# Kernel tuning notes

Hardware: AMD Instinct MI355X
Metric: run time of the kernel (lower is better)

## Reference

```python
import jax, jax.numpy as jnp
import numpy as np

HEADS = 16
DIM_HEAD = 128
SCALE = DIM_HEAD ** -0.5


def rotate_half(x):
    # x: (..., d) with d even; pairs (x1, x2) -> (-x2, x1)
    x = x.reshape(*x.shape[:-1], -1, 2)
    x1, x2 = x[..., 0], x[..., 1]
    return jnp.stack([-x2, x1], axis=-1).reshape(*x.shape[:-2], -1)


def apply_rotary(freqs, t):
    # freqs: (n, d), t: (b, h, n, d)
    cos = jnp.cos(freqs)[None, None]
    sin = jnp.sin(freqs)[None, None]
    return t * cos + rotate_half(t) * sin


def setup_inputs() -> dict:
    key = jax.random.key(0)
    ks = jax.random.split(key, 6)
    b, n, dim = 2, 2048, 2048
    inner = HEADS * DIM_HEAD
    s = dim ** -0.5
    x = jax.random.normal(ks[0], (b, n, dim), dtype=jnp.float32)
    rotary_emb = jax.random.normal(ks[1], (n, DIM_HEAD), dtype=jnp.float32)
    Wq = jax.random.normal(ks[2], (dim, inner), dtype=jnp.float32) * s
    Wkv = jax.random.normal(ks[3], (dim, 2 * inner), dtype=jnp.float32) * s
    Wo = jax.random.normal(ks[4], (inner, dim), dtype=jnp.float32) * s
    bo = jnp.zeros((dim,), dtype=jnp.float32)
    return {"x": x, "rotary_emb": rotary_emb, "Wq": Wq, "Wkv": Wkv, "Wo": Wo, "bo": bo}


def reference(x, rotary_emb, Wq, Wkv, Wo, bo):
    b, n, _ = x.shape
    q = x @ Wq                      # (b, n, inner)
    kv = x @ Wkv                    # (b, n, 2*inner)
    k, v = jnp.split(kv, 2, axis=-1)
    # b n (h d) -> b h n d
    split = lambda t: t.reshape(b, n, HEADS, DIM_HEAD).transpose(0, 2, 1, 3)
    q, k, v = split(q), split(k), split(v)
    q = apply_rotary(rotary_emb, q)
    k = apply_rotary(rotary_emb, k)
    q = q * SCALE
    dots = jnp.einsum('bhid,bhjd->bhij', q, k)
    attn = jax.nn.softmax(dots, axis=-1)
    out = jnp.einsum('bhij,bhjd->bhid', attn, v)
    out = out.transpose(0, 2, 1, 3).reshape(b, n, HEADS * DIM_HEAD)
    return out @ Wo + bo
```

## Files before the change

### kernel.cpp

```cpp
#include <hip/hip_runtime.h>
#include <stdint.h>

typedef __attribute__((ext_vector_type(8))) short s16x8;
typedef __attribute__((ext_vector_type(4))) float f32x4;

#define DEVFN static __device__ __forceinline__

constexpr int   S_LEN = 2048;
constexpr int   DH    = 128;
constexpr int   INNER = 2048;
constexpr float ASCALE = 0.08838834764831845f;

DEVFN float b2f(unsigned short u) {
  union { unsigned int i; float f; } v; v.i = ((unsigned int)u) << 16; return v.f;
}
DEVFN unsigned short f2b(float f) {
  union { float f; unsigned int i; } v; v.f = f;
  unsigned int r = v.i + 0x7fffu + ((v.i >> 16) & 1u);
  return (unsigned short)(r >> 16);
}
DEVFN void async_cp16(const unsigned short* g, unsigned short* l) {
  __builtin_amdgcn_global_load_lds((const __attribute__((address_space(1))) void*)g,
                                   (__attribute__((address_space(3))) void*)l, 16, 0, 0);
}

__global__ __launch_bounds__(256) void cvt_bf16_k(const float* __restrict__ in,
                                                  unsigned short* __restrict__ out) {
  const size_t e = ((size_t)blockIdx.x * 256 + threadIdx.x) * 8;
  const float4 a = *(const float4*)(in + e);
  const float4 b = *(const float4*)(in + e + 4);
  union { s16x8 v; unsigned short u[8]; } o;
  o.u[0] = f2b(a.x); o.u[1] = f2b(a.y); o.u[2] = f2b(a.z); o.u[3] = f2b(a.w);
  o.u[4] = f2b(b.x); o.u[5] = f2b(b.y); o.u[6] = f2b(b.z); o.u[7] = f2b(b.w);
  *(s16x8*)(out + e) = o.v;
}

__global__ __launch_bounds__(256) void rot_cs_k(const float* __restrict__ rot,
                                                float2* __restrict__ cst) {
  const int idx = blockIdx.x * 256 + threadIdx.x;
  const float f = rot[idx];
  float s, c;
  __sincosf(f, &s, &c);
  cst[idx] = make_float2(c, s);
}

__global__ __launch_bounds__(256) void transpose_cvt_k(const float* __restrict__ in,
                                                       unsigned short* __restrict__ out,
                                                       int R, int C) {
  __shared__ __align__(16) unsigned short tile[64][72];
  const int t  = threadIdx.x;
  const int lr = t >> 3;
  const int lc = (t & 7) << 3;
  const size_t ibase = (size_t)blockIdx.y * 64 * C + (size_t)blockIdx.x * 64;
#pragma unroll
  for (int rr = 0; rr < 64; rr += 32) {
    const float* p = in + ibase + (size_t)(rr + lr) * C + lc;
    const float4 a = *(const float4*)p;
    const float4 b = *(const float4*)(p + 4);
    unsigned short* tp = &tile[rr + lr][lc];
    tp[0] = f2b(a.x); tp[1] = f2b(a.y); tp[2] = f2b(a.z); tp[3] = f2b(a.w);
    tp[4] = f2b(b.x); tp[5] = f2b(b.y); tp[6] = f2b(b.z); tp[7] = f2b(b.w);
  }
  __syncthreads();
  const size_t obase = (size_t)blockIdx.x * 64 * R + (size_t)blockIdx.y * 64;
#pragma unroll
  for (int rr = 0; rr < 64; rr += 32) {
    int oc = rr + lr;
    union { s16x8 v; unsigned short s[8]; } u;
#pragma unroll
    for (int j = 0; j < 8; ++j) u.s[j] = tile[lc + j][oc];
    *(s16x8*)(out + obase + (size_t)oc * R + lc) = u.v;
  }
}

template <int EPI>
__global__ __launch_bounds__(256) void gemm_bt(
    const unsigned short* __restrict__ A,
    const unsigned short* __restrict__ Bt,
    unsigned short* __restrict__ out0,
    unsigned short* __restrict__ out1,
    unsigned short* __restrict__ out2,
    float* __restrict__ outf,
    const float* __restrict__ biasf,
    const float2* __restrict__ rotcs,
    int M, int N, int K) {
  __shared__ __align__(16) unsigned short smem[16384];
  unsigned short* As = smem;
  unsigned short* Bs = smem + 8192;
  const int tid  = threadIdx.x;
  const int wave = tid >> 6, lane = tid & 63;
  const int wm = wave & 1, wn = wave >> 1;
  const int quad = lane >> 4, l15 = lane & 15;
  const int l7 = l15 & 7;
  const int m0 = blockIdx.x * 128, n0 = blockIdx.y * 128;

  f32x4 acc[4][4];
#pragma unroll
  for (int i = 0; i < 4; ++i)
#pragma unroll
    for (int j = 0; j < 4; ++j) acc[i][j] = {0.f, 0.f, 0.f, 0.f};

  const int lrow = lane >> 3;
  const int lchk = (lane & 7) ^ (lrow & 7);
  const unsigned short* a_g = A  + (size_t)(m0 + wave * 32 + lrow) * K + (lchk << 3);
  const unsigned short* b_g = Bt + (size_t)(n0 + wave * 32 + lrow) * K + (lchk << 3);
  unsigned short* As_w = As + (wave * 32) * 64;
  unsigned short* Bs_w = Bs + (wave * 32) * 64;

  for (int k0 = 0; k0 < K; k0 += 64) {
    __syncthreads();
#pragma unroll
    for (int t = 0; t < 4; ++t) {
      async_cp16(a_g + k0 + (size_t)(t * 8) * K, As_w + t * 8 * 64);
      async_cp16(b_g + k0 + (size_t)(t * 8) * K, Bs_w + t * 8 * 64);
    }
    __syncthreads();
#pragma unroll
    for (int ks = 0; ks < 2; ++ks) {
      s16x8 af[4], bfr[4];
#pragma unroll
      for (int mi = 0; mi < 4; ++mi)
        af[mi] = *(const s16x8*)(As + (wm * 64 + mi * 16 + l15) * 64 + (((ks * 4 + quad) ^ l7) << 3));
#pragma unroll
      for (int ni = 0; ni < 4; ++ni)
        bfr[ni] = *(const s16x8*)(Bs + (wn * 64 + ni * 16 + l15) * 64 + (((ks * 4 + quad) ^ l7) << 3));
#pragma unroll
      for (int mi = 0; mi < 4; ++mi)
#pragma unroll
        for (int ni = 0; ni < 4; ++ni)
          acc[mi][ni] = __builtin_amdgcn_mfma_f32_16x16x32_bf16(af[mi], bfr[ni], acc[mi][ni], 0, 0, 0);
    }
  }

  if constexpr (EPI == 1) {
#pragma unroll
    for (int mi = 0; mi < 4; ++mi)
#pragma unroll
      for (int ni = 0; ni < 4; ++ni)
#pragma unroll
        for (int r = 0; r < 4; ++r) {
          const int gm = m0 + wm * 64 + mi * 16 + quad * 4 + r;
          const int gn = n0 + wn * 64 + ni * 16 + l15;
          outf[(size_t)gm * N + gn] = acc[mi][ni][r] + biasf[gn];
        }
  } else {
    __syncthreads();
    const int b     = m0 >> 11;
    const int ibase = m0 & 2047;
    if (n0 < 2 * INNER) {
      const bool isq = (n0 < INNER);
      const int h = (n0 & (INNER - 1)) >> 7;
#pragma unroll
      for (int mi = 0; mi < 4; ++mi)
#pragma unroll
        for (int ni = 0; ni < 4; ++ni) {
          const int dd = wn * 64 + ni * 16 + l15;
          const int ch = dd >> 3;
#pragma unroll
          for (int r = 0; r < 4; ++r) {
            const int il = wm * 64 + mi * 16 + quad * 4 + r;
            const float v  = acc[mi][ni][r];
            const float vp = __shfl_xor(v, 1);
            const float2 cs = rotcs[(size_t)(ibase + il) * 128 + dd];
            float rv = (dd & 1) ? fmaf(v, cs.x,  vp * cs.y)
                                : fmaf(v, cs.x, -vp * cs.y);
            if (isq) rv *= ASCALE;
            smem[il * 128 + ((ch ^ (il & 7)) << 3) + (dd & 7)] = f2b(rv);
          }
        }
      __syncthreads();
      unsigned short* outp = (isq ? out0 : out1) +
                             ((size_t)((b << 4) + h) * S_LEN + ibase) * DH;
#pragma unroll
      for (int it = 0; it < 8; ++it) {
        const int f  = it * 256 + tid;
        const int il = f >> 4, ch = f & 15;
        s16x8 vv = *(const s16x8*)(smem + il * 128 + ((ch ^ (il & 7)) << 3));
        *(s16x8*)(outp + (size_t)il * DH + (ch << 3)) = vv;
      }
    } else {
      const int h = (n0 - 2 * INNER) >> 7;
#pragma unroll
      for (int mi = 0; mi < 4; ++mi)
#pragma unroll
        for (int ni = 0; ni < 4; ++ni) {
          const int dd = wn * 64 + ni * 16 + l15;
#pragma unroll
          for (int r = 0; r < 4; ++r) {
            const int il = wm * 64 + mi * 16 + quad * 4 + r;
            smem[dd * 128 + (((il >> 3) ^ (dd & 7)) << 3) + (il & 7)] = f2b(acc[mi][ni][r]);
          }
        }
      __syncthreads();
      unsigned short* outp = out2 + (size_t)((b << 4) + h) * DH * S_LEN + ibase;
#pragma unroll
      for (int it = 0; it < 8; ++it) {
        const int f  = it * 256 + tid;
        const int dd = f >> 4, ch = f & 15;
        s16x8 vv = *(const s16x8*)(smem + dd * 128 + ((ch ^ (dd & 7)) << 3));
        *(s16x8*)(outp + (size_t)dd * S_LEN + (ch << 3)) = vv;
      }
    }
  }
}

DEVFN void stage_tile(const unsigned short* kh, const unsigned short* vh,
                      int j0, unsigned short* KsB, unsigned short* VsB, int tid) {
#pragma unroll
  for (int v = 0; v < 4; ++v) {
    const int off = v * 2048 + tid * 8;
    const int kr = off >> 7;
    const int kc = (((off & 127) >> 3) ^ (kr & 7)) << 3;
    async_cp16(kh + (size_t)(j0 + kr) * DH + kc, KsB + off);
    const int vr = off >> 6;
    const int vc = (((off & 63) >> 3) ^ (vr & 7)) << 3;
    async_cp16(vh + (size_t)vr * S_LEN + j0 + vc, VsB + off);
  }
}

__global__ __launch_bounds__(256, 2) void flash_attn(
    const unsigned short* __restrict__ q,
    const unsigned short* __restrict__ k,
    const unsigned short* __restrict__ vt,
    unsigned short* __restrict__ aout) {
  __shared__ __align__(16) unsigned short Ks[2][64 * 128];
  __shared__ __align__(16) unsigned short Vs[2][128 * 64];
  __shared__ __align__(16) unsigned short Ps[4][32 * 64];
  const int tid = threadIdx.x;
  const int w = tid >> 6, lane = tid & 63;
  const int quad = lane >> 4, l15 = lane & 15;
  const int l7 = l15 & 7;

  const int lin  = blockIdx.y * 16 + blockIdx.x;
  const int xcd  = lin & 7, slot = lin >> 3;
  const int bh   = (xcd << 2) + (slot >> 4);
  const int i0   = (slot & 15) * 128;

  const unsigned short* qh = q  + (size_t)bh * S_LEN * DH;
  const unsigned short* kh = k  + (size_t)bh * S_LEN * DH;
  const unsigned short* vh = vt + (size_t)bh * DH * S_LEN;

  s16x8 qf[2][4];
#pragma unroll
  for (int mi = 0; mi < 2; ++mi)
#pragma unroll
    for (int ks = 0; ks < 4; ++ks)
      qf[mi][ks] = *(const s16x8*)(qh + (size_t)(i0 + w * 32 + mi * 16 + l15) * DH + ks * 32 + quad * 8);

  f32x4 oacc[2][8];
#pragma unroll
  for (int mi = 0; mi < 2; ++mi)
#pragma unroll
    for (int ni = 0; ni < 8; ++ni) oacc[mi][ni] = {0.f, 0.f, 0.f, 0.f};
  float mrun[2][4], lrun[2][4];
#pragma unroll
  for (int mi = 0; mi < 2; ++mi)
#pragma unroll
    for (int r = 0; r < 4; ++r) { mrun[mi][r] = -1e30f; lrun[mi][r] = 0.f; }

  unsigned short* Pw = Ps[w];

  stage_tile(kh, vh, 0, Ks[0], Vs[0], tid);
  __syncthreads();
  int cur = 0;

  for (int j0 = 0; j0 < S_LEN; j0 += 64) {
    if (j0 + 64 < S_LEN)
      stage_tile(kh, vh, j0 + 64, Ks[cur ^ 1], Vs[cur ^ 1], tid);
    const unsigned short* Ksc = Ks[cur];
    const unsigned short* Vsc = Vs[cur];

    f32x4 sacc[2][4];
#pragma unroll
    for (int mi = 0; mi < 2; ++mi)
#pragma unroll
      for (int ni = 0; ni < 4; ++ni) sacc[mi][ni] = {0.f, 0.f, 0.f, 0.f};
#pragma unroll
    for (int ks = 0; ks < 4; ++ks) {
      s16x8 kb[4];
#pragma unroll
      for (int ni = 0; ni < 4; ++ni)
        kb[ni] = *(const s16x8*)(Ksc + (ni * 16 + l15) * 128 + (((ks * 4 + quad) ^ l7) << 3));
#pragma unroll
      for (int mi = 0; mi < 2; ++mi)
#pragma unroll
        for (int ni = 0; ni < 4; ++ni)
          sacc[mi][ni] = __builtin_amdgcn_mfma_f32_16x16x32_bf16(qf[mi][ks], kb[ni], sacc[mi][ni], 0, 0, 0);
    }

    float al[2][4];
    int anyresc = 0;
#pragma unroll
    for (int mi = 0; mi < 2; ++mi)
#pragma unroll
      for (int r = 0; r < 4; ++r) {
        float v = fmaxf(fmaxf(sacc[mi][0][r], sacc[mi][1][r]),
                        fmaxf(sacc[mi][2][r], sacc[mi][3][r]));
        v = fmaxf(v, __shfl_xor(v, 1));
        v = fmaxf(v, __shfl_xor(v, 2));
        v = fmaxf(v, __shfl_xor(v, 4));
        v = fmaxf(v, __shfl_xor(v, 8));
        const float mo   = mrun[mi][r];
        const int   resc = v > mo + 8.f;
        const float mnew = resc ? v : mo;
        const float a    = resc ? __expf(mo - v) : 1.f;
        mrun[mi][r] = mnew;
        al[mi][r]   = a;
        anyresc |= resc;
        float s0 = 0.f;
#pragma unroll
        for (int ni = 0; ni < 4; ++ni) {
          float p = __expf(sacc[mi][ni][r] - mnew);
          sacc[mi][ni][r] = p;
          s0 += p;
        }
        lrun[mi][r] = lrun[mi][r] * a + s0;
      }
    if (__any(anyresc)) {
#pragma unroll
      for (int mi = 0; mi < 2; ++mi)
#pragma unroll
        for (int ni = 0; ni < 8; ++ni)
#pragma unroll
          for (int r = 0; r < 4; ++r) oacc[mi][ni][r] *= al[mi][r];
    }

#pragma unroll
    for (int mi = 0; mi < 2; ++mi)
#pragma unroll
      for (int ni = 0; ni < 4; ++ni) {
        const int col = ni * 16 + l15;
        const int ch  = col >> 3;
#pragma unroll
        for (int r = 0; r < 4; ++r) {
          const int row = mi * 16 + quad * 4 + r;
          Pw[row * 64 + ((ch ^ (row & 7)) << 3) + (col & 7)] = f2b(sacc[mi][ni][r]);
        }
      }
    __threadfence_block();

#pragma unroll
    for (int ks = 0; ks < 2; ++ks) {
      const int swz = ((ks * 4 + quad) ^ l7) << 3;
      s16x8 pf[2];
#pragma unroll
      for (int mi = 0; mi < 2; ++mi)
        pf[mi] = *(const s16x8*)(Pw + (mi * 16 + l15) * 64 + swz);
#pragma unroll
      for (int ni = 0; ni < 8; ++ni) {
        s16x8 vb = *(const s16x8*)(Vsc + (ni * 16 + l15) * 64 + swz);
#pragma unroll
        for (int mi = 0; mi < 2; ++mi)
          oacc[mi][ni] = __builtin_amdgcn_mfma_f32_16x16x32_bf16(pf[mi], vb, oacc[mi][ni], 0, 0, 0);
      }
    }

    __syncthreads();
    cur ^= 1;
  }

  const int b = bh >> 4, h = bh & 15;
#pragma unroll
  for (int mi = 0; mi < 2; ++mi)
#pragma unroll
    for (int r = 0; r < 4; ++r) {
      float l = lrun[mi][r];
      l += __shfl_xor(l, 1);
      l += __shfl_xor(l, 2);
      l += __shfl_xor(l, 4);
      l += __shfl_xor(l, 8);
      const float inv = 1.0f / l;
      const int i = i0 + w * 32 + mi * 16 + quad * 4 + r;
#pragma unroll
      for (int ni = 0; ni < 8; ++ni) {
        const int dd = ni * 16 + l15;
        aout[((size_t)b * S_LEN + i) * INNER + h * DH + dd] = f2b(oacc[mi][ni][r] * inv);
      }
    }
}

extern "C" void kernel_launch(void* const* d_in, const int* in_sizes, int n_in,
                              void* d_out, int out_size, void* d_ws, size_t ws_size,
                              hipStream_t stream) {
  const float* x   = (const float*)d_in[0];
  const float* rot = (const float*)d_in[1];
  const float* Wq  = (const float*)d_in[2];
  const float* Wkv = (const float*)d_in[3];
  const float* Wo  = (const float*)d_in[4];
  const float* bo  = (const float*)d_in[5];
  float* out = (float*)d_out;

  unsigned short* ws = (unsigned short*)d_ws;
  unsigned short* wt  = ws;
  unsigned short* wot = wt  + (size_t)6144 * 2048;
  unsigned short* qb  = wot + (size_t)2048 * 2048;
  unsigned short* kb  = qb  + (size_t)32 * 2048 * 128;
  unsigned short* vtb = kb  + (size_t)32 * 2048 * 128;
  unsigned short* xb  = vtb + (size_t)32 * 2048 * 128;
  unsigned short* att = wt;

  float2* cst = (float2*)d_out;

  rot_cs_k<<<dim3(1024), 256, 0, stream>>>(rot, cst);
  cvt_bf16_k<<<dim3(4096), 256, 0, stream>>>(x, xb);
  transpose_cvt_k<<<dim3(32, 32), 256, 0, stream>>>(Wq,  wt, 2048, 2048);
  transpose_cvt_k<<<dim3(64, 32), 256, 0, stream>>>(Wkv, wt + (size_t)2048 * 2048, 2048, 4096);
  transpose_cvt_k<<<dim3(32, 32), 256, 0, stream>>>(Wo,  wot, 2048, 2048);

  gemm_bt<0><<<dim3(32, 48), 256, 0, stream>>>(xb, wt, qb, kb, vtb, nullptr, nullptr, cst, 4096, 6144, 2048);
  flash_attn<<<dim3(16, 32), 256, 0, stream>>>(qb, kb, vtb, att);
  gemm_bt<1><<<dim3(32, 16), 256, 0, stream>>>(att, wot, nullptr, nullptr, nullptr, out, bo, nullptr, 4096, 2048, 2048);
}
```

Measured before the change: 438.1 us.

## Add 256x256-tile pipelined QKV GEMM with block swizzle and async double buffering

Replaces the 128x128 QKV projection GEMM with a dedicated 512-thread kernel that computes 256x256 output tiles. It double-buffers A and B in 128 KB of LDS via async global-to-LDS copies, interleaves prefetch with MFMA phases under explicit barriers, raises wave priority around the MFMAs, and remaps block indices for L2 locality. The larger tile cuts global traffic per FLOP. In exchange it uses much more LDS and registers, which lowers occupancy, and it launches only 384 blocks, which may leave compute units unevenly loaded. The rotary and transposed-V epilogues are adapted to span two heads per tile.

```diff
diff --git a/kernel.cpp b/kernel.cpp
--- a/kernel.cpp
+++ b/kernel.cpp
@@ -73,16 +73,170 @@
   }
 }
 
-template <int EPI>
-__global__ __launch_bounds__(256) void gemm_bt(
+__global__ __launch_bounds__(512, 2) void gemm256_qkv(
     const unsigned short* __restrict__ A,
     const unsigned short* __restrict__ Bt,
     unsigned short* __restrict__ out0,
     unsigned short* __restrict__ out1,
     unsigned short* __restrict__ out2,
+    const float2* __restrict__ rotcs) {
+  constexpr int K = 2048, NT = 32;
+  __shared__ __align__(16) unsigned short smem[65536];
+  const int tid = threadIdx.x;
+  const int wid = tid >> 6, lane = tid & 63;
+  const int wm = wid >> 2, wn = wid & 3;
+  const int quad = lane >> 4, l15 = lane & 15, l7 = l15 & 7;
+
+  const int lin = blockIdx.x;
+  const int logical = (lin & 7) * 48 + (lin >> 3);
+  const int m0 = (logical & 15) * 256;
+  const int n0 = (logical >> 4) * 256;
+
+  const int r0 = tid >> 3, c0 = tid & 7;
+
+  f32x4 acc[8][4];
+#pragma unroll
+  for (int i = 0; i < 8; ++i)
+#pragma unroll
+    for (int j = 0; j < 4; ++j) acc[i][j] = {0.f, 0.f, 0.f, 0.f};
+
+  auto stageA = [&](int t, int h) {
+#pragma unroll
+    for (int s = 0; s < 2; ++s) {
+      const int r = s * 64 + r0;
+      async_cp16(A + (size_t)(m0 + h * 128 + r) * K + t * 64 + ((c0 ^ (r0 & 7)) << 3),
+                 smem + ((t & 1) * 2 + h) * 8192 + s * 4096 + tid * 8);
+    }
+  };
+  auto stageB = [&](int t, int h) {
+#pragma unroll
+    for (int s = 0; s < 2; ++s) {
+      const int r = s * 64 + r0;
+      async_cp16(Bt + (size_t)(n0 + h * 128 + r) * K + t * 64 + ((c0 ^ (r0 & 7)) << 3),
+                 smem + 32768 + ((t & 1) * 2 + h) * 8192 + s * 4096 + tid * 8);
+    }
+  };
+
+  stageA(0, 0); stageA(0, 1); stageB(0, 0); stageB(0, 1);
+  stageB(1, 0); stageB(1, 1);
+  asm volatile("s_waitcnt vmcnt(4)" ::: "memory");
+  __builtin_amdgcn_s_barrier();
+
+#pragma unroll 2
+  for (int t = 0; t < NT; ++t) {
+    const int cur = t & 1;
+    const unsigned short* Ab = smem + (cur * 2 + wm) * 8192;
+    const unsigned short* Bb = smem + 32768 + (cur * 2 + (wn >> 1)) * 8192;
+    const int bln = (wn & 1) * 64;
+    s16x8 bf[4][2];
+#pragma unroll
+    for (int p = 0; p < 4; ++p) {
+      s16x8 af[2][2];
+#pragma unroll
+      for (int j = 0; j < 2; ++j)
+#pragma unroll
+        for (int kk = 0; kk < 2; ++kk)
+          af[j][kk] = *(const s16x8*)(Ab + ((2 * p + j) * 16 + l15) * 64 + (((kk * 4 + quad) ^ l7) << 3));
+      if (p == 0) {
+#pragma unroll
+        for (int nf = 0; nf < 4; ++nf)
+#pragma unroll
+          for (int kk = 0; kk < 2; ++kk)
+            bf[nf][kk] = *(const s16x8*)(Bb + (bln + nf * 16 + l15) * 64 + (((kk * 4 + quad) ^ l7) << 3));
+      }
+      if (p == 0 && t + 1 < NT) stageA(t + 1, 0);
+      if (p == 1 && t + 1 < NT) stageA(t + 1, 1);
+      if (p == 2 && t + 2 < NT) stageB(t + 2, 0);
+      if (p == 3 && t + 2 < NT) stageB(t + 2, 1);
+      __builtin_amdgcn_s_barrier();
+      asm volatile("s_waitcnt lgkmcnt(0)" ::: "memory");
+      __builtin_amdgcn_sched_barrier(0);
+      __builtin_amdgcn_s_setprio(1);
+#pragma unroll
+      for (int kk = 0; kk < 2; ++kk)
+#pragma unroll
+        for (int j = 0; j < 2; ++j)
+#pragma unroll
+          for (int nf = 0; nf < 4; ++nf)
+            acc[2 * p + j][nf] = __builtin_amdgcn_mfma_f32_16x16x32_bf16(af[j][kk], bf[nf][kk], acc[2 * p + j][nf], 0, 0, 0);
+      __builtin_amdgcn_s_setprio(0);
+      __builtin_amdgcn_sched_barrier(0);
+      if (p == 3) {
+        if (t == NT - 2)      asm volatile("s_waitcnt vmcnt(0)" ::: "memory");
+        else if (t < NT - 2)  asm volatile("s_waitcnt vmcnt(4)" ::: "memory");
+      }
+      __builtin_amdgcn_s_barrier();
+    }
+  }
+
+  __syncthreads();
+  const int b = m0 >> 11, ibase = m0 & 2047;
+  if (n0 < 2 * INNER) {
+    const bool isq = (n0 < INNER);
+    const int hbase = (n0 & (INNER - 1)) >> 7;
+#pragma unroll
+    for (int mf = 0; mf < 8; ++mf)
+#pragma unroll
+      for (int nf = 0; nf < 4; ++nf) {
+        const int jl = wn * 64 + nf * 16 + l15;
+        const int dd = jl & 127;
+        const int cl = jl >> 3;
+#pragma unroll
+        for (int r = 0; r < 4; ++r) {
+          const int il = wm * 128 + mf * 16 + quad * 4 + r;
+          const float v  = acc[mf][nf][r];
+          const float vp = __shfl_xor(v, 1);
+          const float2 cs = rotcs[(size_t)(ibase + il) * 128 + dd];
+          float rv = (dd & 1) ? fmaf(v, cs.x,  vp * cs.y)
+                              : fmaf(v, cs.x, -vp * cs.y);
+          if (isq) rv *= ASCALE;
+          smem[il * 256 + ((cl ^ (il & 7)) << 3) + (jl & 7)] = f2b(rv);
+        }
+      }
+    __syncthreads();
+    unsigned short* outp = (isq ? out0 : out1) +
+                           ((size_t)((b << 4) + hbase) * S_LEN + ibase) * DH;
+#pragma unroll
+    for (int it = 0; it < 16; ++it) {
+      const int f  = it * 512 + tid;
+      const int il = f >> 5, cl = f & 31;
+      s16x8 vv = *(const s16x8*)(smem + il * 256 + ((cl ^ (il & 7)) << 3));
+      const int hh = cl >> 4, dd0 = (cl & 15) << 3;
+      *(s16x8*)(outp + (size_t)hh * S_LEN * DH + (size_t)il * DH + dd0) = vv;
+    }
+  } else {
+    const int hbase = (n0 - 2 * INNER) >> 7;
+#pragma unroll
+    for (int mf = 0; mf < 8; ++mf)
+#pragma unroll
+      for (int nf = 0; nf < 4; ++nf) {
+        const int jl = wn * 64 + nf * 16 + l15;
+#pragma unroll
+        for (int r = 0; r < 4; ++r) {
+          const int il = wm * 128 + mf * 16 + quad * 4 + r;
+          const int ci = il >> 3;
+          smem[jl * 256 + ((ci ^ (jl & 7)) << 3) + (il & 7)] = f2b(acc[mf][nf][r]);
+        }
+      }
+    __syncthreads();
+    unsigned short* outp = out2 + (size_t)((b << 4) + hbase) * DH * S_LEN + ibase;
+#pragma unroll
+    for (int it = 0; it < 16; ++it) {
+      const int f  = it * 512 + tid;
+      const int jl = f >> 5, ci = f & 31;
+      s16x8 vv = *(const s16x8*)(smem + jl * 256 + ((ci ^ (jl & 7)) << 3));
+      const int hh = jl >> 7, dd = jl & 127;
+      *(s16x8*)(outp + (size_t)hh * DH * S_LEN + (size_t)dd * S_LEN + (ci << 3)) = vv;
+    }
+  }
+}
+
+template <int EPI>
+__global__ __launch_bounds__(256) void gemm_bt(
+    const unsigned short* __restrict__ A,
+    const unsigned short* __restrict__ Bt,
     float* __restrict__ outf,
     const float* __restrict__ biasf,
-    const float2* __restrict__ rotcs,
     int M, int N, int K) {
   __shared__ __align__(16) unsigned short smem[16384];
   unsigned short* As = smem;
@@ -132,76 +286,16 @@
     }
   }
 
-  if constexpr (EPI == 1) {
-#pragma unroll
-    for (int mi = 0; mi < 4; ++mi)
-#pragma unroll
-      for (int ni = 0; ni < 4; ++ni)
-#pragma unroll
-        for (int r = 0; r < 4; ++r) {
-          const int gm = m0 + wm * 64 + mi * 16 + quad * 4 + r;
-          const int gn = n0 + wn * 64 + ni * 16 + l15;
-          outf[(size_t)gm * N + gn] = acc[mi][ni][r] + biasf[gn];
-        }
-  } else {
-    __syncthreads();
-    const int b     = m0 >> 11;
-    const int ibase = m0 & 2047;
-    if (n0 < 2 * INNER) {
-      const bool isq = (n0 < INNER);
-      const int h = (n0 & (INNER - 1)) >> 7;
-#pragma unroll
-      for (int mi = 0; mi < 4; ++mi)
-#pragma unroll
-        for (int ni = 0; ni < 4; ++ni) {
-          const int dd = wn * 64 + ni * 16 + l15;
-          const int ch = dd >> 3;
-#pragma unroll
-          for (int r = 0; r < 4; ++r) {
-            const int il = wm * 64 + mi * 16 + quad * 4 + r;
-            const float v  = acc[mi][ni][r];
-            const float vp = __shfl_xor(v, 1);
-            const float2 cs = rotcs[(size_t)(ibase + il) * 128 + dd];
-            float rv = (dd & 1) ? fmaf(v, cs.x,  vp * cs.y)
-                                : fmaf(v, cs.x, -vp * cs.y);
-            if (isq) rv *= ASCALE;
-            smem[il * 128 + ((ch ^ (il & 7)) << 3) + (dd & 7)] = f2b(rv);
-          }
-        }
-      __syncthreads();
-      unsigned short* outp = (isq ? out0 : out1) +
-                             ((size_t)((b << 4) + h) * S_LEN + ibase) * DH;
-#pragma unroll
-      for (int it = 0; it < 8; ++it) {
-        const int f  = it * 256 + tid;
-        const int il = f >> 4, ch = f & 15;
-        s16x8 vv = *(const s16x8*)(smem + il * 128 + ((ch ^ (il & 7)) << 3));
-        *(s16x8*)(outp + (size_t)il * DH + (ch << 3)) = vv;
-      }
-    } else {
-      const int h = (n0 - 2 * INNER) >> 7;
-#pragma unroll
-      for (int mi = 0; mi < 4; ++mi)
-#pragma unroll
-        for (int ni = 0; ni < 4; ++ni) {
-          const int dd = wn * 64 + ni * 16 + l15;
-#pragma unroll
-          for (int r = 0; r < 4; ++r) {
-            const int il = wm * 64 + mi * 16 + quad * 4 + r;
-            smem[dd * 128 + (((il >> 3) ^ (dd & 7)) << 3) + (il & 7)] = f2b(acc[mi][ni][r]);
-          }
-        }
-      __syncthreads();
-      unsigned short* outp = out2 + (size_t)((b << 4) + h) * DH * S_LEN + ibase;
-#pragma unroll
-      for (int it = 0; it < 8; ++it) {
-        const int f  = it * 256 + tid;
-        const int dd = f >> 4, ch = f & 15;
-        s16x8 vv = *(const s16x8*)(smem + dd * 128 + ((ch ^ (dd & 7)) << 3));
-        *(s16x8*)(outp + (size_t)dd * S_LEN + (ch << 3)) = vv;
-      }
-    }
-  }
+#pragma unroll
+  for (int mi = 0; mi < 4; ++mi)
+#pragma unroll
+    for (int ni = 0; ni < 4; ++ni)
+#pragma unroll
+      for (int r = 0; r < 4; ++r) {
+        const int gm = m0 + wm * 64 + mi * 16 + quad * 4 + r;
+        const int gn = n0 + wn * 64 + ni * 16 + l15;
+        outf[(size_t)gm * N + gn] = acc[mi][ni][r] + biasf[gn];
+      }
 }
 
 DEVFN void stage_tile(const unsigned short* kh, const unsigned short* vh,
@@ -407,7 +501,7 @@
   transpose_cvt_k<<<dim3(64, 32), 256, 0, stream>>>(Wkv, wt + (size_t)2048 * 2048, 2048, 4096);
   transpose_cvt_k<<<dim3(32, 32), 256, 0, stream>>>(Wo,  wot, 2048, 2048);
 
-  gemm_bt<0><<<dim3(32, 48), 256, 0, stream>>>(xb, wt, qb, kb, vtb, nullptr, nullptr, cst, 4096, 6144, 2048);
+  gemm256_qkv<<<dim3(384), 512, 0, stream>>>(xb, wt, qb, kb, vtb, cst);
   flash_attn<<<dim3(16, 32), 256, 0, stream>>>(qb, kb, vtb, att);
-  gemm_bt<1><<<dim3(32, 16), 256, 0, stream>>>(att, wot, nullptr, nullptr, nullptr, out, bo, nullptr, 4096, 2048, 2048);
-}
+  gemm_bt<1><<<dim3(32, 16), 256, 0, stream>>>(att, wot, out, bo, 4096, 2048, 2048);
+}
```

Result: no change. 432.4 us (-1.3%).
